# Kernel optimization log

Measured on AMD Instinct MI355X. Metric: run time of the kernel, lower is better.

## Reference

```python
import jax, jax.numpy as jnp
import numpy as np

B, T, A, IN = 128, 512, 2, 192
N_SESS, RDIM, OUT = 512, 64, 256


def setup_inputs() -> dict:
    key = jax.random.key(0)
    k1, k2, k3, k4 = jax.random.split(key, 4)
    state_in = jax.random.normal(k1, (B, T, A, IN), dtype=jnp.float32)
    session = jax.random.randint(k2, (B,), 0, N_SESS, dtype=jnp.int64)
    # kaiming-uniform-like init scale, exact distribution irrelevant for correctness baseline
    unique_readin = jax.random.normal(k3, (N_SESS, IN, RDIM), dtype=jnp.float32) * (1.0 / np.sqrt(IN))
    project = jax.random.normal(k4, (RDIM, OUT), dtype=jnp.float32) * (1.0 / np.sqrt(RDIM))
    return {"state_in": state_in, "session": session,
            "unique_readin": unique_readin, "project": project}


def reference(state_in, session, unique_readin, project):
    # gather per-sample readin matrices: [B, IN, RDIM]
    readin_matrix = unique_readin[session]
    # btai,bih->btah : per-sample matmul over the input-feature axis
    h = jnp.einsum('btai,bih->btah', state_in, readin_matrix)
    # low-rank compression projection to model dim: [B, T, A, OUT]
    out = jnp.matmul(h, project)
    return out
```

## Files before the change

kernel.cpp:

```cpp
#include <hip/hip_runtime.h>
#include <hip/hip_bf16.h>
#include <stdint.h>


typedef short    bf16x8 __attribute__((ext_vector_type(8)));
typedef float    f32x4  __attribute__((ext_vector_type(4)));
typedef uint32_t u32x4  __attribute__((ext_vector_type(4)));

#define NB    128
#define MPB   1024
#define INF   192
#define RDIM  64
#define OUTF  256

#define WAIT_VM4()   asm volatile("s_waitcnt vmcnt(4)" ::: "memory")
#define WAIT_VM0()   asm volatile("s_waitcnt vmcnt(0)" ::: "memory")
#define WAIT_LGKM0() asm volatile("s_waitcnt lgkmcnt(0)" ::: "memory")

__device__ __forceinline__ uint16_t f2bf(float f) {
    union { float f; uint32_t u; } v; v.f = f;
    return (uint16_t)((v.u + 0x7fffu + ((v.u >> 16) & 1u)) >> 16);
}
__device__ __forceinline__ uint32_t pack2(float a, float b) {
    return (uint32_t)f2bf(a) | ((uint32_t)f2bf(b) << 16);
}
__device__ __forceinline__ bf16x8 cvt8(f32x4 a, f32x4 b) {
    union { __hip_bfloat162 h2[4]; bf16x8 h; } r;
    r.h2[0] = __float22bfloat162_rn({a[0], a[1]});
    r.h2[1] = __float22bfloat162_rn({a[2], a[3]});
    r.h2[2] = __float22bfloat162_rn({b[0], b[1]});
    r.h2[3] = __float22bfloat162_rn({b[2], b[3]});
    return r.h;
}
__device__ __forceinline__ void gl_lds16(const void* g, void* l) {
    auto gp = (const __attribute__((address_space(1))) uint32_t*)(uintptr_t)g;
    auto lp = (__attribute__((address_space(3))) uint32_t*)(uintptr_t)l;
    __builtin_amdgcn_global_load_lds(gp, lp, 16, 0, 0);
}

__global__ __launch_bounds__(256, 2) void fused_gemm(
    const float* __restrict__ X,
    const int*   __restrict__ session,
    const float* __restrict__ readin,
    const float* __restrict__ project,
    float*       __restrict__ Y)
{
    __shared__ __attribute__((aligned(16))) uint8_t arena[81920];

    const int bid0 = blockIdx.x;
    const int bid  = ((bid0 & 7) << 8) | (bid0 >> 3);
    const int b  = bid >> 4;
    const int mt = (bid >> 1) & 7;
    const int nt = bid & 1;
    const int t  = threadIdx.x, l = t & 63, w = t >> 6;
    const int lr = l & 15, lk = l >> 4;

    const float* Xb = X + ((size_t)b * MPB + mt * 128) * INF;
    float*       Yb = Y + ((size_t)b * MPB + mt * 128) * OUTF + nt * 128;

    {
        uint16_t* Rl = (uint16_t*)arena;
        uint16_t* Pl = (uint16_t*)(arena + 49152);
        const float* Rg = readin + (size_t)session[b] * (INF * RDIM);

#pragma unroll
        for (int c = 0; c < 3; ++c) {
            int idx = c * 4096 + t * 16;
            int row = idx >> 6;
            int kg0 = (idx & 63) >> 3;
            f32x4 v0 = *(const f32x4*)(Rg + idx);
            f32x4 v1 = *(const f32x4*)(Rg + idx + 4);
            f32x4 v2 = *(const f32x4*)(Rg + idx + 8);
            f32x4 v3 = *(const f32x4*)(Rg + idx + 12);
            u32x4 d0, d1;
            d0[0] = pack2(v0[0], v0[1]); d0[1] = pack2(v0[2], v0[3]);
            d0[2] = pack2(v1[0], v1[1]); d0[3] = pack2(v1[2], v1[3]);
            d1[0] = pack2(v2[0], v2[1]); d1[1] = pack2(v2[2], v2[3]);
            d1[2] = pack2(v3[0], v3[1]); d1[3] = pack2(v3[2], v3[3]);
            *(u32x4*)&Rl[row * 64 + (((kg0    ) ^ (row & 7)) << 3)] = d0;
            *(u32x4*)&Rl[row * 64 + (((kg0 + 1) ^ (row & 7)) << 3)] = d1;
        }
        {
            int h  = t >> 2;
            int og = (t & 3) * 32;
            const float* Pg = project + (size_t)h * OUTF + nt * 128 + og;
#pragma unroll
            for (int q = 0; q < 8; ++q) {
                f32x4 v = *(const f32x4*)(Pg + q * 4);
#pragma unroll
                for (int e = 0; e < 4; ++e) {
                    int o = og + q * 4 + e;
                    Pl[o * 64 + (((h >> 3) ^ (o & 7)) << 3) + (h & 7)] = f2bf(v[e]);
                }
            }
        }
        __syncthreads();

        const int wm = w >> 1, wn = w & 1;
        f32x4 acc[4][6];
#pragma unroll
        for (int m = 0; m < 4; ++m)
#pragma unroll
            for (int n = 0; n < 6; ++n) acc[m][n] = f32x4{0.f, 0.f, 0.f, 0.f};

#pragma unroll
        for (int kk = 0; kk < 2; ++kk) {
            int kg = kk * 4 + lk;
            bf16x8 a[4], bb[6];
#pragma unroll
            for (int m = 0; m < 4; ++m) {
                int row = wm * 64 + m * 16 + lr;
                a[m] = *(const bf16x8*)&Pl[row * 64 + ((kg ^ (row & 7)) << 3)];
            }
#pragma unroll
            for (int n = 0; n < 6; ++n) {
                int col = wn * 96 + n * 16 + lr;
                bb[n] = *(const bf16x8*)&Rl[col * 64 + ((kg ^ (col & 7)) << 3)];
            }
#pragma unroll
            for (int m = 0; m < 4; ++m)
#pragma unroll
                for (int n = 0; n < 6; ++n)
                    acc[m][n] = __builtin_amdgcn_mfma_f32_16x16x32_bf16(
                        a[m], bb[n], acc[m][n], 0, 0, 0);
        }
        __syncthreads();

        uint16_t* Bs16 = (uint16_t*)arena;
#pragma unroll
        for (int m = 0; m < 4; ++m) {
            int o0 = wm * 64 + m * 16 + lk * 4;
#pragma unroll
            for (int n = 0; n < 6; ++n) {
                int i = wn * 96 + n * 16 + lr;
#pragma unroll
                for (int j = 0; j < 4; ++j)
                    Bs16[((i >> 3) * 128 + (o0 + j)) * 8 + (i & 7)]
                        = f2bf(acc[m][n][j]);
            }
        }
        __syncthreads();
    }

    uint8_t* Ab = arena + 49152 + w * 8192;
    const float* Aw = Xb + (size_t)(w * 32) * INF;

    int asrc[4];
#pragma unroll
    for (int c = 0; c < 4; ++c) {
        int i   = c * 64 + l;
        int row = i >> 3;
        int kq  = (i & 7) ^ (row & 7);
        asrc[c] = row * INF + kq * 4;
    }
    auto stage = [&](int kk, int buf) {
#pragma unroll
        for (int c = 0; c < 4; ++c)
            gl_lds16(Aw + asrc[c] + kk * 32, Ab + buf * 4096 + c * 1024);
    };

    stage(0, 0);
    stage(1, 1);

    f32x4 acc[2][8];
#pragma unroll
    for (int m = 0; m < 2; ++m)
#pragma unroll
        for (int n = 0; n < 8; ++n) acc[m][n] = f32x4{0.f, 0.f, 0.f, 0.f};

    const int a0s = ((2 * lk)     ^ (lr & 7)) << 4;
    const int a1s = ((2 * lk + 1) ^ (lr & 7)) << 4;

#pragma unroll
    for (int kk = 0; kk < 6; ++kk) {
        if (kk < 5) { WAIT_VM4(); } else { WAIT_VM0(); }
        __builtin_amdgcn_sched_barrier(0);

        const uint8_t* Abuf = Ab + (kk & 1) * 4096;
        bf16x8 af[2], bfr[8];
#pragma unroll
        for (int m = 0; m < 2; ++m) {
            const uint8_t* p = Abuf + (m * 16 + lr) * 128;
            f32x4 lo = *(const f32x4*)(p + a0s);
            f32x4 hi = *(const f32x4*)(p + a1s);
            af[m] = cvt8(lo, hi);
        }
#pragma unroll
        for (int n = 0; n < 8; ++n)
            bfr[n] = *(const bf16x8*)(arena
                        + (((kk * 4 + lk) * 128 + n * 16 + lr) << 4));

        WAIT_LGKM0();
        __builtin_amdgcn_sched_barrier(0);
        if (kk < 4) stage(kk + 2, kk & 1);

#pragma unroll
        for (int m = 0; m < 2; ++m)
#pragma unroll
            for (int n = 0; n < 8; ++n)
                acc[m][n] = __builtin_amdgcn_mfma_f32_16x16x32_bf16(
                    af[m], bfr[n], acc[m][n], 0, 0, 0);
    }

#pragma unroll
    for (int m = 0; m < 2; ++m) {
        int r0 = w * 32 + m * 16 + lk * 4;
#pragma unroll
        for (int n = 0; n < 8; ++n) {
            int c0 = n * 16 + lr;
#pragma unroll
            for (int j = 0; j < 4; ++j)
                Yb[(size_t)(r0 + j) * OUTF + c0] = acc[m][n][j];
        }
    }
}

extern "C" void kernel_launch(void* const* d_in, const int* in_sizes, int n_in,
                              void* d_out, int out_size, void* d_ws, size_t ws_size,
                              hipStream_t stream) {
    (void)in_sizes; (void)n_in; (void)out_size; (void)d_ws; (void)ws_size;
    const float* state   = (const float*)d_in[0];
    const int*   session = (const int*)  d_in[1];
    const float* readin  = (const float*)d_in[2];
    const float* project = (const float*)d_in[3];
    float*       out     = (float*)d_out;

    hipLaunchKernelGGL(fused_gemm, dim3(2048), dim3(256), 0, stream,
                       state, session, readin, project, out);
}
```

Measured before the change: 51.25 us.

## Overlap X prefetch with weight fusion and vectorize output stores via transposed MFMA

The first two X tile stages are now issued before the fused weight (readin×project) computation, so the global loads overlap the prologue GEMM. The readin matrix is read straight from global into MFMA fragments rather than staged through LDS, and the fused weight is written to LDS with packed 8-byte stores. The main MFMA operands are swapped so each lane holds four consecutive output columns, which lets results go out as 16-byte vector stores instead of scalar strided ones. The prologue weight GEMM is still recomputed per block, and the direct global readin loads may be less coalesced.

Result: slower. 61.59 us (+20.2%).

```diff
diff --git a/kernel.cpp b/kernel.cpp
--- a/kernel.cpp
+++ b/kernel.cpp
@@ -5,6 +5,7 @@
 
 typedef short    bf16x8 __attribute__((ext_vector_type(8)));
 typedef float    f32x4  __attribute__((ext_vector_type(4)));
+typedef uint32_t u32x2  __attribute__((ext_vector_type(2)));
 typedef uint32_t u32x4  __attribute__((ext_vector_type(4)));
 
 #define NB    128
@@ -58,93 +59,8 @@
     const float* Xb = X + ((size_t)b * MPB + mt * 128) * INF;
     float*       Yb = Y + ((size_t)b * MPB + mt * 128) * OUTF + nt * 128;
 
-    {
-        uint16_t* Rl = (uint16_t*)arena;
-        uint16_t* Pl = (uint16_t*)(arena + 49152);
-        const float* Rg = readin + (size_t)session[b] * (INF * RDIM);
-
-#pragma unroll
-        for (int c = 0; c < 3; ++c) {
-            int idx = c * 4096 + t * 16;
-            int row = idx >> 6;
-            int kg0 = (idx & 63) >> 3;
-            f32x4 v0 = *(const f32x4*)(Rg + idx);
-            f32x4 v1 = *(const f32x4*)(Rg + idx + 4);
-            f32x4 v2 = *(const f32x4*)(Rg + idx + 8);
-            f32x4 v3 = *(const f32x4*)(Rg + idx + 12);
-            u32x4 d0, d1;
-            d0[0] = pack2(v0[0], v0[1]); d0[1] = pack2(v0[2], v0[3]);
-            d0[2] = pack2(v1[0], v1[1]); d0[3] = pack2(v1[2], v1[3]);
-            d1[0] = pack2(v2[0], v2[1]); d1[1] = pack2(v2[2], v2[3]);
-            d1[2] = pack2(v3[0], v3[1]); d1[3] = pack2(v3[2], v3[3]);
-            *(u32x4*)&Rl[row * 64 + (((kg0    ) ^ (row & 7)) << 3)] = d0;
-            *(u32x4*)&Rl[row * 64 + (((kg0 + 1) ^ (row & 7)) << 3)] = d1;
-        }
-        {
-            int h  = t >> 2;
-            int og = (t & 3) * 32;
-            const float* Pg = project + (size_t)h * OUTF + nt * 128 + og;
-#pragma unroll
-            for (int q = 0; q < 8; ++q) {
-                f32x4 v = *(const f32x4*)(Pg + q * 4);
-#pragma unroll
-                for (int e = 0; e < 4; ++e) {
-                    int o = og + q * 4 + e;
-                    Pl[o * 64 + (((h >> 3) ^ (o & 7)) << 3) + (h & 7)] = f2bf(v[e]);
-                }
-            }
-        }
-        __syncthreads();
-
-        const int wm = w >> 1, wn = w & 1;
-        f32x4 acc[4][6];
-#pragma unroll
-        for (int m = 0; m < 4; ++m)
-#pragma unroll
-            for (int n = 0; n < 6; ++n) acc[m][n] = f32x4{0.f, 0.f, 0.f, 0.f};
-
-#pragma unroll
-        for (int kk = 0; kk < 2; ++kk) {
-            int kg = kk * 4 + lk;
-            bf16x8 a[4], bb[6];
-#pragma unroll
-            for (int m = 0; m < 4; ++m) {
-                int row = wm * 64 + m * 16 + lr;
-                a[m] = *(const bf16x8*)&Pl[row * 64 + ((kg ^ (row & 7)) << 3)];
-            }
-#pragma unroll
-            for (int n = 0; n < 6; ++n) {
-                int col = wn * 96 + n * 16 + lr;
-                bb[n] = *(const bf16x8*)&Rl[col * 64 + ((kg ^ (col & 7)) << 3)];
-            }
-#pragma unroll
-            for (int m = 0; m < 4; ++m)
-#pragma unroll
-                for (int n = 0; n < 6; ++n)
-                    acc[m][n] = __builtin_amdgcn_mfma_f32_16x16x32_bf16(
-                        a[m], bb[n], acc[m][n], 0, 0, 0);
-        }
-        __syncthreads();
-
-        uint16_t* Bs16 = (uint16_t*)arena;
-#pragma unroll
-        for (int m = 0; m < 4; ++m) {
-            int o0 = wm * 64 + m * 16 + lk * 4;
-#pragma unroll
-            for (int n = 0; n < 6; ++n) {
-                int i = wn * 96 + n * 16 + lr;
-#pragma unroll
-                for (int j = 0; j < 4; ++j)
-                    Bs16[((i >> 3) * 128 + (o0 + j)) * 8 + (i & 7)]
-                        = f2bf(acc[m][n][j]);
-            }
-        }
-        __syncthreads();
-    }
-
     uint8_t* Ab = arena + 49152 + w * 8192;
     const float* Aw = Xb + (size_t)(w * 32) * INF;
-
     int asrc[4];
 #pragma unroll
     for (int c = 0; c < 4; ++c) {
@@ -162,6 +78,70 @@
     stage(0, 0);
     stage(1, 1);
 
+    {
+        uint16_t* Pl = (uint16_t*)arena;
+        const float* Rg = readin + (size_t)session[b] * (INF * RDIM);
+
+        {
+            int h  = t >> 2;
+            int og = (t & 3) * 32;
+            const float* Pg = project + (size_t)h * OUTF + nt * 128 + og;
+#pragma unroll
+            for (int q = 0; q < 8; ++q) {
+                f32x4 v = *(const f32x4*)(Pg + q * 4);
+#pragma unroll
+                for (int e = 0; e < 4; ++e) {
+                    int o = og + q * 4 + e;
+                    Pl[o * 64 + (((h >> 3) ^ (o & 7)) << 3) + (h & 7)] = f2bf(v[e]);
+                }
+            }
+        }
+        __syncthreads();
+
+        f32x4 wacc[3][8];
+#pragma unroll
+        for (int ii = 0; ii < 3; ++ii)
+#pragma unroll
+            for (int ob = 0; ob < 8; ++ob) wacc[ii][ob] = f32x4{0.f,0.f,0.f,0.f};
+
+#pragma unroll
+        for (int kk = 0; kk < 2; ++kk) {
+            bf16x8 rf[3];
+#pragma unroll
+            for (int ii = 0; ii < 3; ++ii) {
+                const float* p = Rg + (size_t)((w * 3 + ii) * 16 + lr) * RDIM
+                               + kk * 32 + lk * 8;
+                rf[ii] = cvt8(*(const f32x4*)p, *(const f32x4*)(p + 4));
+            }
+            const int kg = kk * 4 + lk;
+#pragma unroll
+            for (int ob = 0; ob < 8; ++ob) {
+                int o = ob * 16 + lr;
+                bf16x8 pf = *(const bf16x8*)&Pl[o * 64 + ((kg ^ (o & 7)) << 3)];
+#pragma unroll
+                for (int ii = 0; ii < 3; ++ii)
+                    wacc[ii][ob] = __builtin_amdgcn_mfma_f32_16x16x32_bf16(
+                        rf[ii], pf, wacc[ii][ob], 0, 0, 0);
+            }
+        }
+        __syncthreads();
+
+        uint8_t* BsB = arena;
+#pragma unroll
+        for (int ii = 0; ii < 3; ++ii) {
+            int ib = w * 3 + ii;
+            int ubase = (ib * 2 + (lk >> 1)) * 128;
+#pragma unroll
+            for (int ob = 0; ob < 8; ++ob) {
+                u32x2 d;
+                d[0] = pack2(wacc[ii][ob][0], wacc[ii][ob][1]);
+                d[1] = pack2(wacc[ii][ob][2], wacc[ii][ob][3]);
+                *(u32x2*)&BsB[(size_t)(ubase + ob * 16 + lr) * 16 + (lk & 1) * 8] = d;
+            }
+        }
+        __syncthreads();
+    }
+
     f32x4 acc[2][8];
 #pragma unroll
     for (int m = 0; m < 2; ++m)
@@ -199,19 +179,15 @@
 #pragma unroll
             for (int n = 0; n < 8; ++n)
                 acc[m][n] = __builtin_amdgcn_mfma_f32_16x16x32_bf16(
-                    af[m], bfr[n], acc[m][n], 0, 0, 0);
+                    bfr[n], af[m], acc[m][n], 0, 0, 0);
     }
 
 #pragma unroll
     for (int m = 0; m < 2; ++m) {
-        int r0 = w * 32 + m * 16 + lk * 4;
-#pragma unroll
-        for (int n = 0; n < 8; ++n) {
-            int c0 = n * 16 + lr;
-#pragma unroll
-            for (int j = 0; j < 4; ++j)
-                Yb[(size_t)(r0 + j) * OUTF + c0] = acc[m][n][j];
-        }
+        float* yr = Yb + (size_t)(w * 32 + m * 16 + lr) * OUTF + lk * 4;
+#pragma unroll
+        for (int n = 0; n < 8; ++n)
+            *(f32x4*)(yr + n * 16) = acc[m][n];
     }
 }
 
```

## Load A tiles directly into registers instead of LDS staging, raise occupancy

Applied to the files above, without the earlier changes.

Replaces the global-to-LDS async staging of the fp32 activation tile with inline-asm global_load_dwordx4 straight into registers, double-buffered in two register sets. This removes the A-tile region from shared memory, shrinking LDS from 80KB to 48KB, and launch bounds are raised to allow three blocks per CU. The intent is to eliminate LDS round-trips for A and improve latency hiding through occupancy. The trade-off is higher register pressure under the tighter bound, and it relies on manual vmcnt waits being correct for asm loads the compiler cannot track.

Measured after the change: 58.53 us. 14.2% more time.

```diff
diff --git a/kernel.cpp b/kernel.cpp
--- a/kernel.cpp
+++ b/kernel.cpp
@@ -15,7 +15,6 @@
 
 #define WAIT_VM4()   asm volatile("s_waitcnt vmcnt(4)" ::: "memory")
 #define WAIT_VM0()   asm volatile("s_waitcnt vmcnt(0)" ::: "memory")
-#define WAIT_LGKM0() asm volatile("s_waitcnt lgkmcnt(0)" ::: "memory")
 
 __device__ __forceinline__ uint16_t f2bf(float f) {
     union { float f; uint32_t u; } v; v.f = f;
@@ -32,20 +31,19 @@
     r.h2[3] = __float22bfloat162_rn({b[2], b[3]});
     return r.h;
 }
-__device__ __forceinline__ void gl_lds16(const void* g, void* l) {
-    auto gp = (const __attribute__((address_space(1))) uint32_t*)(uintptr_t)g;
-    auto lp = (__attribute__((address_space(3))) uint32_t*)(uintptr_t)l;
-    __builtin_amdgcn_global_load_lds(gp, lp, 16, 0, 0);
-}
-
-__global__ __launch_bounds__(256, 2) void fused_gemm(
+__device__ __forceinline__ void gload4(f32x4& d, const float* p) {
+    asm volatile("global_load_dwordx4 %0, %1, off"
+                 : "=&v"(d) : "v"(p));
+}
+
+__global__ __launch_bounds__(256, 3) void fused_gemm(
     const float* __restrict__ X,
     const int*   __restrict__ session,
     const float* __restrict__ readin,
     const float* __restrict__ project,
     float*       __restrict__ Y)
 {
-    __shared__ __attribute__((aligned(16))) uint8_t arena[81920];
+    __shared__ __attribute__((aligned(16))) uint8_t arena[49152];
 
     const int bid0 = blockIdx.x;
     const int bid  = ((bid0 & 7) << 8) | (bid0 >> 3);
@@ -60,7 +58,7 @@
 
     {
         uint16_t* Rl = (uint16_t*)arena;
-        uint16_t* Pl = (uint16_t*)(arena + 49152);
+        uint16_t* Pl = (uint16_t*)(arena + 24576);
         const float* Rg = readin + (size_t)session[b] * (INF * RDIM);
 
 #pragma unroll
@@ -142,25 +140,19 @@
         __syncthreads();
     }
 
-    uint8_t* Ab = arena + 49152 + w * 8192;
-    const float* Aw = Xb + (size_t)(w * 32) * INF;
-
-    int asrc[4];
-#pragma unroll
-    for (int c = 0; c < 4; ++c) {
-        int i   = c * 64 + l;
-        int row = i >> 3;
-        int kq  = (i & 7) ^ (row & 7);
-        asrc[c] = row * INF + kq * 4;
-    }
-    auto stage = [&](int kk, int buf) {
-#pragma unroll
-        for (int c = 0; c < 4; ++c)
-            gl_lds16(Aw + asrc[c] + kk * 32, Ab + buf * 4096 + c * 1024);
+    const float* Aw = Xb + (size_t)(w * 32 + lr) * INF + lk * 8;
+
+    f32x4 pa0[4], pa1[4];
+    auto issueA = [&](int kk, f32x4* pa) {
+        const float* p = Aw + kk * 32;
+        gload4(pa[0], p);
+        gload4(pa[1], p + 4);
+        gload4(pa[2], p + 16 * INF);
+        gload4(pa[3], p + 16 * INF + 4);
     };
 
-    stage(0, 0);
-    stage(1, 1);
+    issueA(0, pa0);
+    issueA(1, pa1);
 
     f32x4 acc[2][8];
 #pragma unroll
@@ -168,31 +160,23 @@
 #pragma unroll
         for (int n = 0; n < 8; ++n) acc[m][n] = f32x4{0.f, 0.f, 0.f, 0.f};
 
-    const int a0s = ((2 * lk)     ^ (lr & 7)) << 4;
-    const int a1s = ((2 * lk + 1) ^ (lr & 7)) << 4;
-
 #pragma unroll
     for (int kk = 0; kk < 6; ++kk) {
-        if (kk < 5) { WAIT_VM4(); } else { WAIT_VM0(); }
-        __builtin_amdgcn_sched_barrier(0);
-
-        const uint8_t* Abuf = Ab + (kk & 1) * 4096;
-        bf16x8 af[2], bfr[8];
-#pragma unroll
-        for (int m = 0; m < 2; ++m) {
-            const uint8_t* p = Abuf + (m * 16 + lr) * 128;
-            f32x4 lo = *(const f32x4*)(p + a0s);
-            f32x4 hi = *(const f32x4*)(p + a1s);
-            af[m] = cvt8(lo, hi);
-        }
+        bf16x8 bfr[8];
 #pragma unroll
         for (int n = 0; n < 8; ++n)
             bfr[n] = *(const bf16x8*)(arena
                         + (((kk * 4 + lk) * 128 + n * 16 + lr) << 4));
 
-        WAIT_LGKM0();
+        if (kk < 5) { WAIT_VM4(); } else { WAIT_VM0(); }
         __builtin_amdgcn_sched_barrier(0);
-        if (kk < 4) stage(kk + 2, kk & 1);
+
+        f32x4* cur = (kk & 1) ? pa1 : pa0;
+        bf16x8 af[2];
+        af[0] = cvt8(cur[0], cur[1]);
+        af[1] = cvt8(cur[2], cur[3]);
+
+        if (kk < 4) issueA(kk + 2, cur);
 
 #pragma unroll
         for (int m = 0; m < 2; ++m)
```

## Process two 128-row M tiles per block to amortize fused weight precompute

Applied to the files above, without the earlier changes.

Each block now covers 256 rows of M instead of 128, halving the grid to 1024 blocks. The combined readin×project weight matrix is computed once per block and reused across both row tiles, streaming 12 pipelined X stages into two separate accumulator sets. This cuts redundant weight-prologue work and session gathers per output. In exchange it doubles accumulator registers, which could hurt occupancy at the launch bound, and leaves fewer blocks to spread across the CUs.

New measurement: 45.46 us. -11.3%, faster.

```diff
diff --git a/kernel.cpp b/kernel.cpp
--- a/kernel.cpp
+++ b/kernel.cpp
@@ -48,15 +48,15 @@
     __shared__ __attribute__((aligned(16))) uint8_t arena[81920];
 
     const int bid0 = blockIdx.x;
-    const int bid  = ((bid0 & 7) << 8) | (bid0 >> 3);
-    const int b  = bid >> 4;
-    const int mt = (bid >> 1) & 7;
+    const int bid  = ((bid0 & 7) << 7) | (bid0 >> 3);
+    const int b  = bid >> 3;
+    const int mt = (bid >> 1) & 3;
     const int nt = bid & 1;
     const int t  = threadIdx.x, l = t & 63, w = t >> 6;
     const int lr = l & 15, lk = l >> 4;
 
-    const float* Xb = X + ((size_t)b * MPB + mt * 128) * INF;
-    float*       Yb = Y + ((size_t)b * MPB + mt * 128) * OUTF + nt * 128;
+    const float* Xb = X + ((size_t)b * MPB + mt * 256) * INF;
+    float*       Yb = Y + ((size_t)b * MPB + mt * 256) * OUTF + nt * 128;
 
     {
         uint16_t* Rl = (uint16_t*)arena;
@@ -143,8 +143,6 @@
     }
 
     uint8_t* Ab = arena + 49152 + w * 8192;
-    const float* Aw = Xb + (size_t)(w * 32) * INF;
-
     int asrc[4];
 #pragma unroll
     for (int c = 0; c < 4; ++c) {
@@ -153,30 +151,37 @@
         int kq  = (i & 7) ^ (row & 7);
         asrc[c] = row * INF + kq * 4;
     }
-    auto stage = [&](int kk, int buf) {
+    const float* Aw = Xb + (size_t)(w * 32) * INF;
+
+    auto stage = [&](int s, int buf) {
+        const float* src = Aw + (s / 6) * (128 * INF) + (s % 6) * 32;
 #pragma unroll
         for (int c = 0; c < 4; ++c)
-            gl_lds16(Aw + asrc[c] + kk * 32, Ab + buf * 4096 + c * 1024);
+            gl_lds16(src + asrc[c], Ab + buf * 4096 + c * 1024);
     };
 
     stage(0, 0);
     stage(1, 1);
 
-    f32x4 acc[2][8];
+    f32x4 accA[2][8], accB[2][8];
 #pragma unroll
     for (int m = 0; m < 2; ++m)
 #pragma unroll
-        for (int n = 0; n < 8; ++n) acc[m][n] = f32x4{0.f, 0.f, 0.f, 0.f};
+        for (int n = 0; n < 8; ++n) {
+            accA[m][n] = f32x4{0.f, 0.f, 0.f, 0.f};
+            accB[m][n] = f32x4{0.f, 0.f, 0.f, 0.f};
+        }
 
     const int a0s = ((2 * lk)     ^ (lr & 7)) << 4;
     const int a1s = ((2 * lk + 1) ^ (lr & 7)) << 4;
 
 #pragma unroll
-    for (int kk = 0; kk < 6; ++kk) {
-        if (kk < 5) { WAIT_VM4(); } else { WAIT_VM0(); }
+    for (int s = 0; s < 12; ++s) {
+        if (s < 10) { WAIT_VM4(); } else { WAIT_VM0(); }
         __builtin_amdgcn_sched_barrier(0);
 
-        const uint8_t* Abuf = Ab + (kk & 1) * 4096;
+        const uint8_t* Abuf = Ab + (s & 1) * 4096;
+        const int kk = s % 6;
         bf16x8 af[2], bfr[8];
 #pragma unroll
         for (int m = 0; m < 2; ++m) {
@@ -192,14 +197,23 @@
 
         WAIT_LGKM0();
         __builtin_amdgcn_sched_barrier(0);
-        if (kk < 4) stage(kk + 2, kk & 1);
-
-#pragma unroll
-        for (int m = 0; m < 2; ++m)
-#pragma unroll
-            for (int n = 0; n < 8; ++n)
-                acc[m][n] = __builtin_amdgcn_mfma_f32_16x16x32_bf16(
-                    af[m], bfr[n], acc[m][n], 0, 0, 0);
+        if (s < 10) stage(s + 2, s & 1);
+
+        if (s < 6) {
+#pragma unroll
+            for (int m = 0; m < 2; ++m)
+#pragma unroll
+                for (int n = 0; n < 8; ++n)
+                    accA[m][n] = __builtin_amdgcn_mfma_f32_16x16x32_bf16(
+                        af[m], bfr[n], accA[m][n], 0, 0, 0);
+        } else {
+#pragma unroll
+            for (int m = 0; m < 2; ++m)
+#pragma unroll
+                for (int n = 0; n < 8; ++n)
+                    accB[m][n] = __builtin_amdgcn_mfma_f32_16x16x32_bf16(
+                        af[m], bfr[n], accB[m][n], 0, 0, 0);
+        }
     }
 
 #pragma unroll
@@ -209,8 +223,10 @@
         for (int n = 0; n < 8; ++n) {
             int c0 = n * 16 + lr;
 #pragma unroll
-            for (int j = 0; j < 4; ++j)
-                Yb[(size_t)(r0 + j) * OUTF + c0] = acc[m][n][j];
+            for (int j = 0; j < 4; ++j) {
+                Yb[(size_t)(r0 + j) * OUTF + c0]       = accA[m][n][j];
+                Yb[(size_t)(128 + r0 + j) * OUTF + c0] = accB[m][n][j];
+            }
         }
     }
 }
@@ -225,6 +241,6 @@
     const float* project = (const float*)d_in[3];
     float*       out     = (float*)d_out;
 
-    hipLaunchKernelGGL(fused_gemm, dim3(2048), dim3(256), 0, stream,
+    hipLaunchKernelGGL(fused_gemm, dim3(1024), dim3(256), 0, stream,
                        state, session, readin, project, out);
 }
```
